# Kernel optimization log

Hardware: AMD Instinct MI355X
Metric: run time of the kernel (lower is better)

Reference implementation:

```python
import jax, jax.numpy as jnp
import numpy as np

EPS = 1e-6
NEG = -10000.0  # matches _merge_attn_masks neg_inf

def rms(x, w):
    return x * jax.lax.rsqrt(jnp.mean(x * x, axis=-1, keepdims=True) + EPS) * w

def setup_inputs() -> dict:
    key = jax.random.key(0)
    ks = jax.random.split(key, 16)
    B, Tq, Tk, D, H, G, dh, F, E = 4, 1024, 1024, 1024, 16, 4, 64, 4096, 8
    s = 1.0 / np.sqrt(D)
    sf = 1.0 / np.sqrt(F)
    return {
        "x": jax.random.normal(ks[0], (B, Tq, D), jnp.float32),
        "k_ctx": jax.random.normal(ks[1], (B, Tk, G, dh), jnp.float32),
        "v_ctx": jax.random.normal(ks[2], (B, Tk, G, dh), jnp.float32),
        "sa_norm_w": jnp.ones((D,), jnp.float32),
        "w_qkv": jax.random.normal(ks[3], (D, 3 * D), jnp.float32) * s,
        "sa_wout": jax.random.normal(ks[4], (D, D), jnp.float32) * s,
        "ca_norm_w": jnp.ones((D,), jnp.float32),
        "w_q": jax.random.normal(ks[5], (D, D), jnp.float32) * s,
        "ca_wout": jax.random.normal(ks[6], (D, D), jnp.float32) * s,
        "moe_norm_w": jnp.ones((D,), jnp.float32),
        "w_gate": jax.random.normal(ks[7], (D, E), jnp.float32) * s,
        "w1": jax.random.normal(ks[8], (E, D, F), jnp.float32) * s,
        "b1": jnp.zeros((E, F), jnp.float32),
        "w2": jax.random.normal(ks[9], (E, F, D), jnp.float32) * sf,
        "b2": jnp.zeros((E, D), jnp.float32),
    }

def _attn(q, k, v, mask=None):
    # q,k,v: [B,H,T,dh]
    dh = q.shape[-1]
    scores = jnp.einsum("bhqd,bhkd->bhqk", q, k) / jnp.sqrt(jnp.float32(dh))
    if mask is not None:
        scores = scores + mask
    p = jax.nn.softmax(scores, axis=-1)
    return jnp.einsum("bhqk,bhkd->bhqd", p, v)

def reference(x, k_ctx, v_ctx, sa_norm_w, w_qkv, sa_wout, ca_norm_w, w_q, ca_wout,
              moe_norm_w, w_gate, w1, b1, w2, b2):
    B, Tq, D = x.shape
    Tk, G, dh = k_ctx.shape[1], k_ctx.shape[2], k_ctx.shape[3]
    H = 16
    rep = H // G

    # ---- self-attention (causal, pre-norm RMS, residual) ----
    xn = rms(x, sa_norm_w)
    qkv = xn @ w_qkv  # [B,Tq,3D]
    q, k, v = jnp.split(qkv, 3, axis=-1)
    split = lambda t: t.reshape(B, Tq, H, dh).transpose(0, 2, 1, 3)
    i = jnp.arange(Tq)[:, None]
    j = jnp.arange(Tq)[None, :]
    causal = jnp.where(j <= i, 0.0, NEG).astype(jnp.float32)[None, None]
    y = _attn(split(q), split(k), split(v), causal)
    y = y.transpose(0, 2, 1, 3).reshape(B, Tq, D) @ sa_wout
    x = x + y

    # ---- cross-attention GQA ----
    qc = rms(x, ca_norm_w) @ w_q
    qc = qc.reshape(B, Tq, H, dh).transpose(0, 2, 1, 3)
    kk = jnp.repeat(k_ctx, rep, axis=2).transpose(0, 2, 1, 3)  # [B,H,Tk,dh]
    vv = jnp.repeat(v_ctx, rep, axis=2).transpose(0, 2, 1, 3)
    yc = _attn(qc, kk, vv)
    yc = yc.transpose(0, 2, 1, 3).reshape(B, Tq, D) @ ca_wout
    x = x + yc

    # ---- top-1 MoE FFN ----
    xm = rms(x, moe_norm_w)
    gate_scores = jax.nn.softmax(xm @ w_gate, axis=-1)  # [B,T,E]
    top1_idx = jnp.argmax(gate_scores, axis=-1)
    top1_score = jnp.max(gate_scores, axis=-1)
    E = w1.shape[0]
    out = jnp.zeros_like(xm)
    for e in range(E):  # small fixed expert count
        ye = jax.nn.silu(xm @ w1[e] + b1[e]) @ w2[e] + b2[e]
        out = jnp.where((top1_idx == e)[..., None], ye, out)
    out = out * top1_score[..., None]
    return x + out
```

## Files before the change

kernel.cpp:

```cpp
#include <hip/hip_runtime.h>
#include <hip/hip_bf16.h>
#include <stdint.h>

#define B_  4
#define T_  1024
#define D_  1024
#define H_  16
#define DH  64
#define F_  4096
#define E_  8
#define NT  (B_*T_)

typedef float f32x4 __attribute__((ext_vector_type(4)));
typedef short bf16x8 __attribute__((ext_vector_type(8)));
#define MFMA_BF16 __builtin_amdgcn_mfma_f32_16x16x32_bf16

union PK8 { uint32_t u[4]; bf16x8 v; };

#define GL16(gsrc, ldst)                                                      \
  __builtin_amdgcn_global_load_lds(                                           \
      (const __attribute__((address_space(1))) void*)(const void*)(gsrc),     \
      (__attribute__((address_space(3))) void*)(void*)(ldst), 16, 0, 0)

static __device__ __forceinline__ uint16_t f2bf(float f) {
  uint32_t u = __float_as_uint(f);
  u += 0x7FFFu + ((u >> 16) & 1u);
  return (uint16_t)(u >> 16);
}
static __device__ __forceinline__ void unpack8(const uint4 p0, const uint4 p1, bf16x8 &hi, bf16x8 &lo) {
  PK8 H, L;
  H.u[0] = __builtin_amdgcn_perm(p0.y, p0.x, 0x07060302u);
  L.u[0] = __builtin_amdgcn_perm(p0.y, p0.x, 0x05040100u);
  H.u[1] = __builtin_amdgcn_perm(p0.w, p0.z, 0x07060302u);
  L.u[1] = __builtin_amdgcn_perm(p0.w, p0.z, 0x05040100u);
  H.u[2] = __builtin_amdgcn_perm(p1.y, p1.x, 0x07060302u);
  L.u[2] = __builtin_amdgcn_perm(p1.y, p1.x, 0x05040100u);
  H.u[3] = __builtin_amdgcn_perm(p1.w, p1.z, 0x07060302u);
  L.u[3] = __builtin_amdgcn_perm(p1.w, p1.z, 0x05040100u);
  hi = H.v; lo = L.v;
}

__global__ __launch_bounds__(256) void k_pack_t2(const float* __restrict__ in,
                                                 uint16_t* __restrict__ outh, uint16_t* __restrict__ outl,
                                                 int K, int N) {
  __shared__ float t[32][33];
  const size_t mo = (size_t)blockIdx.z * K * N;
  in += mo; outh += mo; outl += mo;
  int n0 = blockIdx.x * 32, k0 = blockIdx.y * 32;
  int tx = threadIdx.x & 31, ty = threadIdx.x >> 5;
#pragma unroll
  for (int i = 0; i < 32; i += 8) t[ty + i][tx] = in[(size_t)(k0 + ty + i) * N + n0 + tx];
  __syncthreads();
#pragma unroll
  for (int i = 0; i < 32; i += 8) {
    float v = t[tx][ty + i];
    uint16_t h = f2bf(v);
    uint16_t l = f2bf(v - __uint_as_float((uint32_t)h << 16));
    size_t o = (size_t)(n0 + ty + i) * K + k0 + tx;
    outh[o] = h; outl[o] = l;
  }
}

__global__ __launch_bounds__(256) void k_bf_t(const float* __restrict__ in, uint16_t* __restrict__ out,
                                              int K, int N) {
  __shared__ float t[64][65];
  const size_t mo = (size_t)blockIdx.z * K * N;
  in += mo; out += mo;
  int n0 = blockIdx.x * 64, k0 = blockIdx.y * 64;
  int tr = threadIdx.x >> 4;
  int tc = (threadIdx.x & 15) * 4;
#pragma unroll
  for (int i = 0; i < 64; i += 16) {
    float4 v = *(const float4*)&in[(size_t)(k0 + tr + i) * N + n0 + tc];
    t[tr + i][tc] = v.x; t[tr + i][tc + 1] = v.y; t[tr + i][tc + 2] = v.z; t[tr + i][tc + 3] = v.w;
  }
  __syncthreads();
#pragma unroll
  for (int i = 0; i < 64; i += 16) {
    int n = tr + i;
    uint16_t b0 = f2bf(t[tc][n]), b1 = f2bf(t[tc + 1][n]);
    uint16_t b2 = f2bf(t[tc + 2][n]), b3 = f2bf(t[tc + 3][n]);
    uint2 wv;
    wv.x = ((uint32_t)b1 << 16) | b0;
    wv.y = ((uint32_t)b3 << 16) | b2;
    *(uint2*)&out[(size_t)(n0 + n) * K + k0 + tc] = wv;
  }
}

__global__ __launch_bounds__(256) void k_t16(const uint16_t* __restrict__ inh, const uint16_t* __restrict__ inl,
                                             uint16_t* __restrict__ outh, uint16_t* __restrict__ outl) {
  __shared__ uint16_t th[64][68], tl[64][68];
  int b = blockIdx.z, t0 = blockIdx.x * 64, c0 = blockIdx.y * 64;
  int tr = threadIdx.x >> 4;
  int tc = (threadIdx.x & 15) * 4;
#pragma unroll
  for (int i = 0; i < 64; i += 16) {
    size_t src = (size_t)(b * T_ + t0 + tr + i) * 3072 + 2048 + c0 + tc;
    *(uint2*)&th[tr + i][tc] = *(const uint2*)&inh[src];
    *(uint2*)&tl[tr + i][tc] = *(const uint2*)&inl[src];
  }
  __syncthreads();
#pragma unroll
  for (int i = 0; i < 64; i += 16) {
    int n = tr + i;
    size_t dst = (size_t)(b * 1024 + c0 + n) * T_ + t0 + tc;
    uint2 ph, pl;
    ph.x = ((uint32_t)th[tc + 1][n] << 16) | th[tc][n];
    ph.y = ((uint32_t)th[tc + 3][n] << 16) | th[tc + 2][n];
    pl.x = ((uint32_t)tl[tc + 1][n] << 16) | tl[tc][n];
    pl.y = ((uint32_t)tl[tc + 3][n] << 16) | tl[tc + 2][n];
    *(uint2*)&outh[dst] = ph;
    *(uint2*)&outl[dst] = pl;
  }
}

__global__ __launch_bounds__(256) void k_packf2(const float* __restrict__ in,
                                                uint16_t* __restrict__ oh, uint16_t* __restrict__ ol) {
  int i = (blockIdx.x * 256 + threadIdx.x) * 4;
  float4 v = *(const float4*)&in[i];
  uint16_t h0 = f2bf(v.x), h1 = f2bf(v.y), h2 = f2bf(v.z), h3 = f2bf(v.w);
  uint2 ph, pl;
  ph.x = ((uint32_t)h1 << 16) | h0;
  ph.y = ((uint32_t)h3 << 16) | h2;
  pl.x = ((uint32_t)f2bf(v.y - __uint_as_float((uint32_t)h1 << 16)) << 16) |
         f2bf(v.x - __uint_as_float((uint32_t)h0 << 16));
  pl.y = ((uint32_t)f2bf(v.w - __uint_as_float((uint32_t)h3 << 16)) << 16) |
         f2bf(v.z - __uint_as_float((uint32_t)h2 << 16));
  *(uint2*)&oh[i] = ph;
  *(uint2*)&ol[i] = pl;
}

__global__ __launch_bounds__(256) void k_tf32(const float* __restrict__ in,
                                              uint16_t* __restrict__ oh, uint16_t* __restrict__ ol) {
  __shared__ float t[32][33];
  int b = blockIdx.z, t0 = blockIdx.x * 32, c0 = blockIdx.y * 32;
  int tx = threadIdx.x & 31, ty = threadIdx.x >> 5;
#pragma unroll
  for (int i = 0; i < 32; i += 8)
    t[ty + i][tx] = in[(size_t)(b * T_ + t0 + ty + i) * 256 + c0 + tx];
  __syncthreads();
#pragma unroll
  for (int i = 0; i < 32; i += 8) {
    float v = t[tx][ty + i];
    uint16_t h = f2bf(v);
    size_t o = (size_t)(b * 256 + c0 + ty + i) * T_ + t0 + tx;
    oh[o] = h;
    ol[o] = f2bf(v - __uint_as_float((uint32_t)h << 16));
  }
}

__global__ __launch_bounds__(256) void k_rms(const float* __restrict__ x, const float* __restrict__ w,
                                             uint16_t* __restrict__ oh, uint16_t* __restrict__ ol,
                                             const float* __restrict__ wg, int* __restrict__ idxp,
                                             float* __restrict__ scb) {
  int row = blockIdx.x;
  const float* xr = x + (size_t)row * D_;
  int t = threadIdx.x;
  float4 xv = *(const float4*)&xr[t * 4];
  float s = xv.x * xv.x + xv.y * xv.y + xv.z * xv.z + xv.w * xv.w;
#pragma unroll
  for (int o = 32; o; o >>= 1) s += __shfl_xor(s, o, 64);
  __shared__ float ps[4];
  __shared__ float ga[4][8];
  if ((t & 63) == 0) ps[t >> 6] = s;
  __syncthreads();
  s = ps[0] + ps[1] + ps[2] + ps[3];
  float sc = 1.0f / sqrtf(s * (1.0f / (float)D_) + 1e-6f);
  float4 wv = *(const float4*)&w[t * 4];
  float o0 = xv.x * sc * wv.x, o1 = xv.y * sc * wv.y, o2 = xv.z * sc * wv.z, o3 = xv.w * sc * wv.w;
  uint16_t h0 = f2bf(o0), h1 = f2bf(o1), h2 = f2bf(o2), h3 = f2bf(o3);
  if (oh) {
    uint2 ph;
    ph.x = ((uint32_t)h1 << 16) | h0;
    ph.y = ((uint32_t)h3 << 16) | h2;
    *(uint2*)&oh[(size_t)row * D_ + t * 4] = ph;
  }
  if (ol) {
    uint16_t l0 = f2bf(o0 - __uint_as_float((uint32_t)h0 << 16));
    uint16_t l1 = f2bf(o1 - __uint_as_float((uint32_t)h1 << 16));
    uint16_t l2 = f2bf(o2 - __uint_as_float((uint32_t)h2 << 16));
    uint16_t l3 = f2bf(o3 - __uint_as_float((uint32_t)h3 << 16));
    uint2 pl;
    pl.x = ((uint32_t)l1 << 16) | l0;
    pl.y = ((uint32_t)l3 << 16) | l2;
    *(uint2*)&ol[(size_t)row * D_ + t * 4] = pl;
  }
  if (wg) {
    float a[8] = {};
    float ov[4] = {o0, o1, o2, o3};
#pragma unroll
    for (int j = 0; j < 4; j++) {
      const float* wr = &wg[(size_t)(t * 4 + j) * 8];
      float4 wa = *(const float4*)wr, wb = *(const float4*)(wr + 4);
      float v = ov[j];
      a[0] += v * wa.x; a[1] += v * wa.y; a[2] += v * wa.z; a[3] += v * wa.w;
      a[4] += v * wb.x; a[5] += v * wb.y; a[6] += v * wb.z; a[7] += v * wb.w;
    }
#pragma unroll
    for (int e = 0; e < 8; e++)
#pragma unroll
      for (int o = 32; o; o >>= 1) a[e] += __shfl_xor(a[e], o, 64);
    if ((t & 63) == 0)
#pragma unroll
      for (int e = 0; e < 8; e++) ga[t >> 6][e] = a[e];
    __syncthreads();
    if (t == 0) {
      float g[8];
#pragma unroll
      for (int e = 0; e < 8; e++) g[e] = ga[0][e] + ga[1][e] + ga[2][e] + ga[3][e];
      int bi = 0; float bv = g[0];
#pragma unroll
      for (int e = 1; e < 8; e++) if (g[e] > bv) { bv = g[e]; bi = e; }
      float se = 0.f;
#pragma unroll
      for (int e = 0; e < 8; e++) se += expf(g[e] - bv);
      idxp[row] = bi;
      scb[row] = 1.0f / se;
    }
  }
}

#define GBM 128
#define GBN 64
__global__ __launch_bounds__(256) void k_gemm_split(const uint16_t* __restrict__ Ahg, const uint16_t* __restrict__ Alg,
                                                    const uint16_t* __restrict__ Whg, const uint16_t* __restrict__ Wlg,
                                                    float* __restrict__ C, const float* __restrict__ res,
                                                    uint16_t* __restrict__ Cph, uint16_t* __restrict__ Cpl,
                                                    int scale_cols, int M, int N, int K) {
  __shared__ uint16_t Ah[2][GBM][32], Al[2][GBM][32];
  __shared__ uint16_t Wh[2][GBN][32], Wl[2][GBN][32];
  int m0 = blockIdx.y * GBM, n0 = blockIdx.x * GBN;
  int tid = threadIdx.x, wv = tid >> 6, ln = tid & 63, mi = ln & 15, b8 = ln >> 4;
  int lr = ln >> 2, lc = ln & 3;
  int cg = lc ^ (lr & 3);
  int rowA = wv * 32 + lr;
  int rowW = wv * 16 + lr;
  const uint16_t* pAh  = Ahg + (size_t)(m0 + rowA) * K + cg * 8;
  const uint16_t* pAl  = Alg + (size_t)(m0 + rowA) * K + cg * 8;
  const uint16_t* pAh2 = pAh + (size_t)16 * K;
  const uint16_t* pAl2 = pAl + (size_t)16 * K;
  const uint16_t* pWh  = Whg + (size_t)(n0 + rowW) * K + cg * 8;
  const uint16_t* pWl  = Wlg + (size_t)(n0 + rowW) * K + cg * 8;
  const int ch8 = (b8 ^ (mi & 3)) * 8;
  f32x4 acc[2][4] = {};

#define STAGE(bf) do {                                                         \
    GL16(pAh,  &Ah[bf][wv * 32][0]);                                           \
    GL16(pAh2, &Ah[bf][wv * 32 + 16][0]);                                      \
    GL16(pAl,  &Al[bf][wv * 32][0]);                                           \
    GL16(pAl2, &Al[bf][wv * 32 + 16][0]);                                      \
    GL16(pWh,  &Wh[bf][wv * 16][0]);                                           \
    GL16(pWl,  &Wl[bf][wv * 16][0]);                                           \
    pAh += 32; pAh2 += 32; pAl += 32; pAl2 += 32; pWh += 32; pWl += 32;        \
  } while (0)

  const int NK = K >> 5;
  STAGE(0);
  __syncthreads();
  int cur = 0;
  for (int t = 0; t < NK; ++t) {
    if (t + 1 < NK) STAGE(cur ^ 1);
    bf16x8 ah[2], al[2], bh[4], bl[4];
#pragma unroll
    for (int fm = 0; fm < 2; fm++) {
      ah[fm] = *(const bf16x8*)&Ah[cur][wv * 32 + fm * 16 + mi][ch8];
      al[fm] = *(const bf16x8*)&Al[cur][wv * 32 + fm * 16 + mi][ch8];
    }
#pragma unroll
    for (int fn = 0; fn < 4; fn++) {
      bh[fn] = *(const bf16x8*)&Wh[cur][fn * 16 + mi][ch8];
      bl[fn] = *(const bf16x8*)&Wl[cur][fn * 16 + mi][ch8];
    }
#pragma unroll
    for (int fm = 0; fm < 2; fm++)
#pragma unroll
      for (int fn = 0; fn < 4; fn++) {
        acc[fm][fn] = MFMA_BF16(al[fm], bh[fn], acc[fm][fn], 0, 0, 0);
        acc[fm][fn] = MFMA_BF16(ah[fm], bl[fn], acc[fm][fn], 0, 0, 0);
        acc[fm][fn] = MFMA_BF16(ah[fm], bh[fn], acc[fm][fn], 0, 0, 0);
      }
    __syncthreads();
    cur ^= 1;
  }
#undef STAGE
#pragma unroll
  for (int fm = 0; fm < 2; fm++)
#pragma unroll
    for (int fn = 0; fn < 4; fn++)
#pragma unroll
      for (int rr = 0; rr < 4; rr++) {
        int row = m0 + wv * 32 + fm * 16 + b8 * 4 + rr;
        int col = n0 + fn * 16 + mi;
        float v = acc[fm][fn][rr];
        size_t o = (size_t)row * N + col;
        if (Cph) {
          if (col < scale_cols) v *= 0.125f;
          uint16_t hv = f2bf(v);
          Cph[o] = hv;
          Cpl[o] = f2bf(v - __uint_as_float((uint32_t)hv << 16));
        } else {
          if (res) v += res[o];
          C[o] = v;
        }
      }
}

template <bool CAUSAL>
__global__ __launch_bounds__(256, 3) void k_fattn(
    const uint16_t* __restrict__ qhg, const uint16_t* __restrict__ qlg, int qs,
    const uint16_t* __restrict__ khg, const uint16_t* __restrict__ klg, int ks_, int khdiv,
    const uint16_t* __restrict__ vhg, const uint16_t* __restrict__ vlg, int nvrows,
    uint16_t* __restrict__ yhg, uint16_t* __restrict__ ylg) {
  __shared__ uint16_t Ksh[64][68], Ksl[64][68];
  __shared__ uint16_t Vsh[64][68], Vsl[64][68];
  __shared__ uint32_t Ps[4][32][36];
  const int h = blockIdx.y, b = blockIdx.z;
  const int qt = CAUSAL ? ((blockIdx.x + h + 2 * b) & 7) : blockIdx.x;
  const int tid = threadIdx.x, wv = tid >> 6, ln = tid & 63, mi = ln & 15, b8 = ln >> 4;
  const int koff = (h / khdiv) * 64;
  const uint16_t* kbh = khg + (size_t)b * T_ * ks_ + koff;
  const uint16_t* kbl = klg + (size_t)b * T_ * ks_ + koff;
  const uint16_t* vbh = vhg + ((size_t)b * nvrows + koff) * T_;
  const uint16_t* vbl = vlg + ((size_t)b * nvrows + koff) * T_;

  bf16x8 qh[2][2], ql[2][2];
#pragma unroll
  for (int u = 0; u < 2; u++)
#pragma unroll
    for (int k2 = 0; k2 < 2; k2++) {
      size_t o = (size_t)(b * T_ + qt * 128 + wv * 32 + u * 16 + mi) * qs + h * 64 + k2 * 32 + b8 * 8;
      qh[u][k2] = *(const bf16x8*)&qhg[o];
      ql[u][k2] = *(const bf16x8*)&qlg[o];
    }

  float m[2][4], l[2][4];
  f32x4 o[2][4] = {};
#pragma unroll
  for (int u = 0; u < 2; u++)
#pragma unroll
    for (int r = 0; r < 4; r++) { m[u][r] = -1e30f; l[u][r] = 0.f; }

  const int nkt = CAUSAL ? (2 * qt + 2) : (T_ / 64);
  for (int kt = 0; kt < nkt; kt++) {
    __syncthreads();
    {
      int rr = tid >> 2, cc = (tid & 3) * 16;
      size_t ko = (size_t)(kt * 64 + rr) * ks_ + cc;
      *(uint4*)&Ksh[rr][cc]     = *(const uint4*)&kbh[ko];
      *(uint4*)&Ksh[rr][cc + 8] = *(const uint4*)&kbh[ko + 8];
      *(uint4*)&Ksl[rr][cc]     = *(const uint4*)&kbl[ko];
      *(uint4*)&Ksl[rr][cc + 8] = *(const uint4*)&kbl[ko + 8];
      size_t vo = (size_t)rr * T_ + kt * 64 + cc;
      *(uint4*)&Vsh[rr][cc]     = *(const uint4*)&vbh[vo];
      *(uint4*)&Vsh[rr][cc + 8] = *(const uint4*)&vbh[vo + 8];
      *(uint4*)&Vsl[rr][cc]     = *(const uint4*)&vbl[vo];
      *(uint4*)&Vsl[rr][cc + 8] = *(const uint4*)&vbl[vo + 8];
    }
    __syncthreads();
#pragma unroll
    for (int s = 0; s < 2; s++) {
      bf16x8 kh[2][2], kl[2][2];
#pragma unroll
      for (int nf = 0; nf < 2; nf++)
#pragma unroll
        for (int k2 = 0; k2 < 2; k2++) {
          int rrow = s * 32 + nf * 16 + mi, ccol = k2 * 32 + b8 * 8;
          kh[nf][k2] = *(const bf16x8*)&Ksh[rrow][ccol];
          kl[nf][k2] = *(const bf16x8*)&Ksl[rrow][ccol];
        }
      f32x4 a[2][2] = {};
#pragma unroll
      for (int u = 0; u < 2; u++)
#pragma unroll
        for (int nf = 0; nf < 2; nf++)
#pragma unroll
          for (int k2 = 0; k2 < 2; k2++) {
            a[u][nf] = MFMA_BF16(ql[u][k2], kh[nf][k2], a[u][nf], 0, 0, 0);
            a[u][nf] = MFMA_BF16(qh[u][k2], kl[nf][k2], a[u][nf], 0, 0, 0);
            a[u][nf] = MFMA_BF16(qh[u][k2], kh[nf][k2], a[u][nf], 0, 0, 0);
          }
      if (CAUSAL && kt >= 2 * qt) {
        int kg = kt * 64 + s * 32 + mi;
#pragma unroll
        for (int u = 0; u < 2; u++) {
          int qg = qt * 128 + wv * 32 + u * 16 + b8 * 4;
#pragma unroll
          for (int r = 0; r < 4; r++) {
            if (kg > qg + r)      a[u][0][r] = -1e30f;
            if (kg + 16 > qg + r) a[u][1][r] = -1e30f;
          }
        }
      }
#pragma unroll
      for (int u = 0; u < 2; u++) {
        float pm[4];
#pragma unroll
        for (int r = 0; r < 4; r++) pm[r] = fmaxf(a[u][0][r], a[u][1][r]);
#pragma unroll
        for (int off = 1; off <= 8; off <<= 1)
#pragma unroll
          for (int r = 0; r < 4; r++) pm[r] = fmaxf(pm[r], __shfl_xor(pm[r], off, 64));
        float sc[4];
#pragma unroll
        for (int r = 0; r < 4; r++) {
          float mn = fmaxf(m[u][r], pm[r]);
          sc[r] = __expf(m[u][r] - mn);
          m[u][r] = mn;
          a[u][0][r] = __expf(a[u][0][r] - mn);
          a[u][1][r] = __expf(a[u][1][r] - mn);
        }
        float rs[4];
#pragma unroll
        for (int r = 0; r < 4; r++) rs[r] = a[u][0][r] + a[u][1][r];
#pragma unroll
        for (int off = 1; off <= 8; off <<= 1)
#pragma unroll
          for (int r = 0; r < 4; r++) rs[r] += __shfl_xor(rs[r], off, 64);
#pragma unroll
        for (int r = 0; r < 4; r++) l[u][r] = l[u][r] * sc[r] + rs[r];
#pragma unroll
        for (int f = 0; f < 4; f++)
#pragma unroll
          for (int r = 0; r < 4; r++) o[u][f][r] *= sc[r];
#pragma unroll
        for (int r = 0; r < 4; r++) {
          uint32_t Hw, Lw;
          asm("v_cvt_pk_bf16_f32 %0, %1, %2" : "=v"(Hw) : "v"(a[u][0][r]), "v"(a[u][1][r]));
          float h0 = __uint_as_float(Hw << 16);
          float h1 = __uint_as_float(Hw & 0xffff0000u);
          float r0 = a[u][0][r] - h0, r1 = a[u][1][r] - h1;
          asm("v_cvt_pk_bf16_f32 %0, %1, %2" : "=v"(Lw) : "v"(r0), "v"(r1));
          Ps[wv][u * 16 + b8 * 4 + r][mi]      = __builtin_amdgcn_perm(Hw, Lw, 0x05040100u);
          Ps[wv][u * 16 + b8 * 4 + r][16 + mi] = __builtin_amdgcn_perm(Hw, Lw, 0x07060302u);
        }
      }
      bf16x8 ph[2], pl[2];
#pragma unroll
      for (int u = 0; u < 2; u++) {
        const uint32_t* p = &Ps[wv][u * 16 + mi][b8 * 8];
        unpack8(*(const uint4*)p, *(const uint4*)(p + 4), ph[u], pl[u]);
      }
#pragma unroll
      for (int f = 0; f < 4; f++) {
        int rrow = f * 16 + mi, ccol = s * 32 + b8 * 8;
        bf16x8 vh = *(const bf16x8*)&Vsh[rrow][ccol];
        bf16x8 vl = *(const bf16x8*)&Vsl[rrow][ccol];
#pragma unroll
        for (int u = 0; u < 2; u++) {
          o[u][f] = MFMA_BF16(pl[u], vh, o[u][f], 0, 0, 0);
          o[u][f] = MFMA_BF16(ph[u], vl, o[u][f], 0, 0, 0);
          o[u][f] = MFMA_BF16(ph[u], vh, o[u][f], 0, 0, 0);
        }
      }
    }
  }
#pragma unroll
  for (int u = 0; u < 2; u++)
#pragma unroll
    for (int r = 0; r < 4; r++) {
      float inv = 1.0f / l[u][r];
      int row = qt * 128 + wv * 32 + u * 16 + b8 * 4 + r;
#pragma unroll
      for (int f = 0; f < 4; f++) {
        size_t idx = (size_t)(b * T_ + row) * D_ + h * 64 + f * 16 + mi;
        float v = o[u][f][r] * inv;
        uint16_t hv = f2bf(v);
        yhg[idx] = hv;
        ylg[idx] = f2bf(v - __uint_as_float((uint32_t)hv << 16));
      }
    }
}

__global__ __launch_bounds__(256) void k_bucket(const int* __restrict__ idx, int* __restrict__ cnt,
                                                int* __restrict__ lists) {
  int tok = blockIdx.x * 256 + threadIdx.x;
  int e = idx[tok];
  int p = atomicAdd(&cnt[e], 1);
  lists[e * NT + p] = tok;
}

__global__ __launch_bounds__(256) void k_moe1(const uint16_t* __restrict__ xmbf, const uint16_t* __restrict__ w1t,
                                              const float* __restrict__ b1, const int* __restrict__ cnt,
                                              const int* __restrict__ lists, uint16_t* __restrict__ hbf) {
  int e = blockIdx.z;
  int c = cnt[e];
  int m0 = blockIdx.y * 64;
  if (m0 >= c) return;
  int n0 = blockIdx.x * 64;
  __shared__ uint16_t As[64][72];
  __shared__ uint16_t Ws[64][72];
  __shared__ int toks[64];
  int tid = threadIdx.x, wv = tid >> 6, ln = tid & 63, mi = ln & 15, b8 = ln >> 4;
  if (tid < 64) toks[tid] = (m0 + tid < c) ? lists[e * NT + m0 + tid] : -1;
  __syncthreads();
  int r = tid >> 2, c16 = (tid & 3) * 16;
  int tk = toks[r];
  const uint16_t* asrc = (tk >= 0) ? (xmbf + (size_t)tk * D_ + c16) : nullptr;
  const uint16_t* wsrc = w1t + (size_t)e * F_ * D_ + (size_t)(n0 + r) * D_ + c16;
  f32x4 acc[4] = {};
  for (int k0 = 0; k0 < D_; k0 += 64) {
    {
      uint4 a0 = make_uint4(0, 0, 0, 0), a1 = make_uint4(0, 0, 0, 0);
      if (asrc) { a0 = *(const uint4*)(asrc + k0); a1 = *(const uint4*)(asrc + k0 + 8); }
      uint4 w0 = *(const uint4*)(wsrc + k0), w1v = *(const uint4*)(wsrc + k0 + 8);
      *(uint4*)&As[r][c16] = a0; *(uint4*)&As[r][c16 + 8] = a1;
      *(uint4*)&Ws[r][c16] = w0; *(uint4*)&Ws[r][c16 + 8] = w1v;
    }
    __syncthreads();
#pragma unroll
    for (int ks = 0; ks < 2; ks++) {
      bf16x8 a = *(const bf16x8*)&As[wv * 16 + mi][ks * 32 + b8 * 8];
#pragma unroll
      for (int fn = 0; fn < 4; fn++) {
        bf16x8 bb = *(const bf16x8*)&Ws[fn * 16 + mi][ks * 32 + b8 * 8];
        acc[fn] = MFMA_BF16(a, bb, acc[fn], 0, 0, 0);
      }
    }
    __syncthreads();
  }
#pragma unroll
  for (int fn = 0; fn < 4; fn++)
#pragma unroll
    for (int rr = 0; rr < 4; rr++) {
      int rt = wv * 16 + b8 * 4 + rr;
      if (m0 + rt < c) {
        int tok = toks[rt];
        int col = n0 + fn * 16 + mi;
        float v = acc[fn][rr] + b1[e * F_ + col];
        v = v / (1.0f + expf(-v));
        hbf[(size_t)tok * F_ + col] = f2bf(v);
      }
    }
}

__global__ __launch_bounds__(256) void k_moe2(const uint16_t* __restrict__ hbf, const uint16_t* __restrict__ w2t,
                                              const float* __restrict__ b2, const float* __restrict__ x2,
                                              const float* __restrict__ sc, const int* __restrict__ cnt,
                                              const int* __restrict__ lists, float* __restrict__ out) {
  int e = blockIdx.z;
  int c = cnt[e];
  int m0 = blockIdx.y * 64;
  if (m0 >= c) return;
  int n0 = blockIdx.x * 64;
  __shared__ uint16_t As[64][72];
  __shared__ uint16_t Ws[64][72];
  __shared__ int toks[64];
  int tid = threadIdx.x, wv = tid >> 6, ln = tid & 63, mi = ln & 15, b8 = ln >> 4;
  if (tid < 64) toks[tid] = (m0 + tid < c) ? lists[e * NT + m0 + tid] : -1;
  __syncthreads();
  int r = tid >> 2, c16 = (tid & 3) * 16;
  int tk = toks[r];
  const uint16_t* asrc = (tk >= 0) ? (hbf + (size_t)tk * F_ + c16) : nullptr;
  const uint16_t* wsrc = w2t + (size_t)e * D_ * F_ + (size_t)(n0 + r) * F_ + c16;
  f32x4 acc[4] = {};
  for (int k0 = 0; k0 < F_; k0 += 64) {
    {
      uint4 a0 = make_uint4(0, 0, 0, 0), a1 = make_uint4(0, 0, 0, 0);
      if (asrc) { a0 = *(const uint4*)(asrc + k0); a1 = *(const uint4*)(asrc + k0 + 8); }
      uint4 w0 = *(const uint4*)(wsrc + k0), w1v = *(const uint4*)(wsrc + k0 + 8);
      *(uint4*)&As[r][c16] = a0; *(uint4*)&As[r][c16 + 8] = a1;
      *(uint4*)&Ws[r][c16] = w0; *(uint4*)&Ws[r][c16 + 8] = w1v;
    }
    __syncthreads();
#pragma unroll
    for (int ks = 0; ks < 2; ks++) {
      bf16x8 a = *(const bf16x8*)&As[wv * 16 + mi][ks * 32 + b8 * 8];
#pragma unroll
      for (int fn = 0; fn < 4; fn++) {
        bf16x8 bb = *(const bf16x8*)&Ws[fn * 16 + mi][ks * 32 + b8 * 8];
        acc[fn] = MFMA_BF16(a, bb, acc[fn], 0, 0, 0);
      }
    }
    __syncthreads();
  }
#pragma unroll
  for (int fn = 0; fn < 4; fn++)
#pragma unroll
    for (int rr = 0; rr < 4; rr++) {
      int rt = wv * 16 + b8 * 4 + rr;
      if (m0 + rt < c) {
        int tok = toks[rt];
        int col = n0 + fn * 16 + mi;
        float v = acc[fn][rr] + b2[e * D_ + col];
        out[(size_t)tok * D_ + col] = x2[(size_t)tok * D_ + col] + sc[tok] * v;
      }
    }
}

extern "C" void kernel_launch(void* const* d_in, const int* in_sizes, int n_in,
                              void* d_out, int out_size, void* d_ws, size_t ws_size,
                              hipStream_t stream) {
  const float* x       = (const float*)d_in[0];
  const float* k_ctx   = (const float*)d_in[1];
  const float* v_ctx   = (const float*)d_in[2];
  const float* sa_nw   = (const float*)d_in[3];
  const float* w_qkv   = (const float*)d_in[4];
  const float* sa_wout = (const float*)d_in[5];
  const float* ca_nw   = (const float*)d_in[6];
  const float* w_q     = (const float*)d_in[7];
  const float* ca_wout = (const float*)d_in[8];
  const float* moe_nw  = (const float*)d_in[9];
  const float* w_gate  = (const float*)d_in[10];
  const float* w1      = (const float*)d_in[11];
  const float* b1      = (const float*)d_in[12];
  const float* w2      = (const float*)d_in[13];
  const float* b2      = (const float*)d_in[14];
  float* out = (float*)d_out;
  (void)in_sizes; (void)n_in; (void)out_size; (void)ws_size;

  char* ws = (char*)d_ws;
  size_t off = 0;
  auto alloc = [&](size_t bytes) { char* p = ws + off; off += (bytes + 255) & ~(size_t)255; return p; };
  uint16_t* xnh   = (uint16_t*)alloc((size_t)NT * D_ * 2);
  uint16_t* xnl   = (uint16_t*)alloc((size_t)NT * D_ * 2);
  uint16_t* yh    = (uint16_t*)alloc((size_t)NT * D_ * 2);
  uint16_t* yl    = (uint16_t*)alloc((size_t)NT * D_ * 2);
  float*    x1    = (float*)alloc((size_t)NT * D_ * 4);
  uint16_t* qkvh  = (uint16_t*)alloc((size_t)NT * 3 * D_ * 2);
  uint16_t* qkvl  = (uint16_t*)alloc((size_t)NT * 3 * D_ * 2);
  float* x2 = (float*)qkvh;
  uint16_t* qch = qkvl;
  uint16_t* qcl = qkvl + (size_t)NT * D_;
  uint16_t* wqkvTh = (uint16_t*)alloc((size_t)D_ * 3 * D_ * 2);
  uint16_t* wqkvTl = (uint16_t*)alloc((size_t)D_ * 3 * D_ * 2);
  uint16_t* sawTh  = (uint16_t*)alloc((size_t)D_ * D_ * 2);
  uint16_t* sawTl  = (uint16_t*)alloc((size_t)D_ * D_ * 2);
  uint16_t* wqTh   = (uint16_t*)alloc((size_t)D_ * D_ * 2);
  uint16_t* wqTl   = (uint16_t*)alloc((size_t)D_ * D_ * 2);
  uint16_t* cawTh  = (uint16_t*)alloc((size_t)D_ * D_ * 2);
  uint16_t* cawTl  = (uint16_t*)alloc((size_t)D_ * D_ * 2);
  uint16_t* w1t   = (uint16_t*)alloc((size_t)E_ * D_ * F_ * 2);
  uint16_t* w2t   = (uint16_t*)alloc((size_t)E_ * D_ * F_ * 2);
  uint16_t* hbf   = (uint16_t*)alloc((size_t)NT * F_ * 2);
  uint16_t* vth   = (uint16_t*)hbf;
  uint16_t* vtl   = vth + (size_t)NT * D_;
  uint16_t* kch   = (uint16_t*)((char*)hbf + (size_t)16 * 1024 * 1024);
  uint16_t* kcl   = (uint16_t*)((char*)hbf + (size_t)18 * 1024 * 1024);
  uint16_t* vcth  = (uint16_t*)((char*)hbf + (size_t)20 * 1024 * 1024);
  uint16_t* vctl  = (uint16_t*)((char*)hbf + (size_t)22 * 1024 * 1024);
  uint16_t* xmbf  = (uint16_t*)alloc((size_t)NT * D_ * 2);
  int*   idx   = (int*)alloc(NT * 4);
  float* scb   = (float*)alloc(NT * 4);
  int*   cnt   = (int*)alloc(256);
  int*   lists = (int*)alloc((size_t)E_ * NT * 4);

  k_pack_t2<<<dim3(3 * D_ / 32, D_ / 32, 1), 256, 0, stream>>>(w_qkv, wqkvTh, wqkvTl, D_, 3 * D_);
  k_pack_t2<<<dim3(D_ / 32, D_ / 32, 1), 256, 0, stream>>>(sa_wout, sawTh, sawTl, D_, D_);
  k_pack_t2<<<dim3(D_ / 32, D_ / 32, 1), 256, 0, stream>>>(w_q, wqTh, wqTl, D_, D_);
  k_pack_t2<<<dim3(D_ / 32, D_ / 32, 1), 256, 0, stream>>>(ca_wout, cawTh, cawTl, D_, D_);
  k_bf_t<<<dim3(F_ / 64, D_ / 64, E_), 256, 0, stream>>>(w1, w1t, D_, F_);
  k_bf_t<<<dim3(D_ / 64, F_ / 64, E_), 256, 0, stream>>>(w2, w2t, F_, D_);
  k_packf2<<<(B_ * T_ * 256) / 1024, 256, 0, stream>>>(k_ctx, kch, kcl);
  k_tf32<<<dim3(T_ / 32, 256 / 32, B_), 256, 0, stream>>>(v_ctx, vcth, vctl);

  k_rms<<<NT, 256, 0, stream>>>(x, sa_nw, xnh, xnl, nullptr, nullptr, nullptr);
  k_gemm_split<<<dim3(3 * D_ / GBN, NT / GBM), 256, 0, stream>>>(xnh, xnl, wqkvTh, wqkvTl, nullptr, nullptr, qkvh, qkvl, 1024, NT, 3 * D_, D_);
  k_t16<<<dim3(T_ / 64, D_ / 64, B_), 256, 0, stream>>>(qkvh, qkvl, vth, vtl);
  k_fattn<true><<<dim3(T_ / 128, H_, B_), 256, 0, stream>>>(qkvh, qkvl, 3072, qkvh + 1024, qkvl + 1024, 3072, 1, vth, vtl, 1024, yh, yl);
  k_gemm_split<<<dim3(D_ / GBN, NT / GBM), 256, 0, stream>>>(yh, yl, sawTh, sawTl, x1, x, nullptr, nullptr, 0, NT, D_, D_);

  k_rms<<<NT, 256, 0, stream>>>(x1, ca_nw, xnh, xnl, nullptr, nullptr, nullptr);
  k_gemm_split<<<dim3(D_ / GBN, NT / GBM), 256, 0, stream>>>(xnh, xnl, wqTh, wqTl, nullptr, nullptr, qch, qcl, 1024, NT, D_, D_);
  k_fattn<false><<<dim3(T_ / 128, H_, B_), 256, 0, stream>>>(qch, qcl, 1024, kch, kcl, 256, 4, vcth, vctl, 256, yh, yl);
  k_gemm_split<<<dim3(D_ / GBN, NT / GBM), 256, 0, stream>>>(yh, yl, cawTh, cawTl, x2, x1, nullptr, nullptr, 0, NT, D_, D_);

  k_rms<<<NT, 256, 0, stream>>>(x2, moe_nw, xmbf, nullptr, w_gate, idx, scb);
  hipMemsetAsync(cnt, 0, 32, stream);
  k_bucket<<<NT / 256, 256, 0, stream>>>(idx, cnt, lists);
  k_moe1<<<dim3(F_ / 64, NT / 64, E_), 256, 0, stream>>>(xmbf, w1t, b1, cnt, lists, hbf);
  k_moe2<<<dim3(D_ / 64, NT / 64, E_), 256, 0, stream>>>(hbf, w2t, b2, x2, scb, cnt, lists, out);
}
```

Before: 845.4 us.

## Merge weight-packing launches and widen MoE up-projection tile to 64x128

Four separate split-bf16 transpose launches become one kernel indexed by blockIdx.z, and the two expert-weight bf16 transposes become another, cutting launch count. The MoE first GEMM moves from a 64x64 to a 64x128 tile. Each wave now computes a 64x32 sub-tile with 4x2 MFMA accumulators and reuses A fragments across two N fragments, which lowers LDS traffic and A reloads per FLOP. The cost is more registers and LDS per block and half as many blocks, which matters when the per-expert token count is small.

```diff
diff --git a/kernel.cpp b/kernel.cpp
--- a/kernel.cpp
+++ b/kernel.cpp
@@ -40,13 +40,21 @@
   hi = H.v; lo = L.v;
 }
 
-__global__ __launch_bounds__(256) void k_pack_t2(const float* __restrict__ in,
-                                                 uint16_t* __restrict__ outh, uint16_t* __restrict__ outl,
-                                                 int K, int N) {
+__global__ __launch_bounds__(256) void k_pack_all(
+    const float* __restrict__ wqkv, const float* __restrict__ saw,
+    const float* __restrict__ wq,   const float* __restrict__ caw,
+    uint16_t* __restrict__ qkvTh, uint16_t* __restrict__ qkvTl,
+    uint16_t* __restrict__ sawTh, uint16_t* __restrict__ sawTl,
+    uint16_t* __restrict__ wqTh,  uint16_t* __restrict__ wqTl,
+    uint16_t* __restrict__ cawTh, uint16_t* __restrict__ cawTl) {
   __shared__ float t[32][33];
-  const size_t mo = (size_t)blockIdx.z * K * N;
-  in += mo; outh += mo; outl += mo;
-  int n0 = blockIdx.x * 32, k0 = blockIdx.y * 32;
+  int z = blockIdx.z;
+  const float* in; uint16_t *oh, *ol; int N, nbase;
+  if (z < 3)       { in = wqkv; oh = qkvTh; ol = qkvTl; N = 3072; nbase = z * 1024; }
+  else if (z == 3) { in = saw;  oh = sawTh; ol = sawTl; N = 1024; nbase = 0; }
+  else if (z == 4) { in = wq;   oh = wqTh;  ol = wqTl;  N = 1024; nbase = 0; }
+  else             { in = caw;  oh = cawTh; ol = cawTl; N = 1024; nbase = 0; }
+  int n0 = nbase + blockIdx.x * 32, k0 = blockIdx.y * 32;
   int tx = threadIdx.x & 31, ty = threadIdx.x >> 5;
 #pragma unroll
   for (int i = 0; i < 32; i += 8) t[ty + i][tx] = in[(size_t)(k0 + ty + i) * N + n0 + tx];
@@ -56,17 +64,25 @@
     float v = t[tx][ty + i];
     uint16_t h = f2bf(v);
     uint16_t l = f2bf(v - __uint_as_float((uint32_t)h << 16));
-    size_t o = (size_t)(n0 + ty + i) * K + k0 + tx;
-    outh[o] = h; outl[o] = l;
-  }
-}
-
-__global__ __launch_bounds__(256) void k_bf_t(const float* __restrict__ in, uint16_t* __restrict__ out,
-                                              int K, int N) {
+    size_t o = (size_t)(n0 + ty + i) * 1024 + k0 + tx;
+    oh[o] = h; ol[o] = l;
+  }
+}
+
+__global__ __launch_bounds__(256) void k_bf_t2(const float* __restrict__ w1, const float* __restrict__ w2,
+                                               uint16_t* __restrict__ w1t, uint16_t* __restrict__ w2t) {
   __shared__ float t[64][65];
-  const size_t mo = (size_t)blockIdx.z * K * N;
+  int z = blockIdx.z;
+  int which = z >> 3, e = z & 7;
+  const float* in = which ? w2 : w1;
+  uint16_t* out = which ? w2t : w1t;
+  int K = which ? F_ : D_, N = which ? D_ : F_;
+  const size_t mo = (size_t)e * (size_t)D_ * F_;
   in += mo; out += mo;
-  int n0 = blockIdx.x * 64, k0 = blockIdx.y * 64;
+  int tile = blockIdx.x;
+  int n0, k0;
+  if (which) { n0 = (tile & 15) * 64; k0 = (tile >> 4) * 64; }
+  else       { n0 = (tile & 63) * 64; k0 = (tile >> 6) * 64; }
   int tr = threadIdx.x >> 4;
   int tc = (threadIdx.x & 15) * 4;
 #pragma unroll
@@ -486,51 +502,62 @@
   int c = cnt[e];
   int m0 = blockIdx.y * 64;
   if (m0 >= c) return;
-  int n0 = blockIdx.x * 64;
+  int n0 = blockIdx.x * 128;
   __shared__ uint16_t As[64][72];
-  __shared__ uint16_t Ws[64][72];
+  __shared__ uint16_t Ws[128][72];
   __shared__ int toks[64];
   int tid = threadIdx.x, wv = tid >> 6, ln = tid & 63, mi = ln & 15, b8 = ln >> 4;
   if (tid < 64) toks[tid] = (m0 + tid < c) ? lists[e * NT + m0 + tid] : -1;
   __syncthreads();
-  int r = tid >> 2, c16 = (tid & 3) * 16;
-  int tk = toks[r];
-  const uint16_t* asrc = (tk >= 0) ? (xmbf + (size_t)tk * D_ + c16) : nullptr;
-  const uint16_t* wsrc = w1t + (size_t)e * F_ * D_ + (size_t)(n0 + r) * D_ + c16;
-  f32x4 acc[4] = {};
+  int ra = tid >> 2, ca = (tid & 3) * 16;
+  int rw = tid >> 1, cw = (tid & 1) * 32;
+  int tk = toks[ra];
+  const uint16_t* asrc = (tk >= 0) ? (xmbf + (size_t)tk * D_ + ca) : nullptr;
+  const uint16_t* wsrc = w1t + (size_t)e * F_ * D_ + (size_t)(n0 + rw) * D_ + cw;
+  f32x4 acc[4][2] = {};
   for (int k0 = 0; k0 < D_; k0 += 64) {
     {
       uint4 a0 = make_uint4(0, 0, 0, 0), a1 = make_uint4(0, 0, 0, 0);
       if (asrc) { a0 = *(const uint4*)(asrc + k0); a1 = *(const uint4*)(asrc + k0 + 8); }
-      uint4 w0 = *(const uint4*)(wsrc + k0), w1v = *(const uint4*)(wsrc + k0 + 8);
-      *(uint4*)&As[r][c16] = a0; *(uint4*)&As[r][c16 + 8] = a1;
-      *(uint4*)&Ws[r][c16] = w0; *(uint4*)&Ws[r][c16 + 8] = w1v;
+      uint4 w0 = *(const uint4*)(wsrc + k0),      w1v = *(const uint4*)(wsrc + k0 + 8);
+      uint4 w2v = *(const uint4*)(wsrc + k0 + 16), w3v = *(const uint4*)(wsrc + k0 + 24);
+      *(uint4*)&As[ra][ca] = a0;      *(uint4*)&As[ra][ca + 8] = a1;
+      *(uint4*)&Ws[rw][cw] = w0;      *(uint4*)&Ws[rw][cw + 8] = w1v;
+      *(uint4*)&Ws[rw][cw + 16] = w2v; *(uint4*)&Ws[rw][cw + 24] = w3v;
     }
     __syncthreads();
 #pragma unroll
     for (int ks = 0; ks < 2; ks++) {
-      bf16x8 a = *(const bf16x8*)&As[wv * 16 + mi][ks * 32 + b8 * 8];
-#pragma unroll
-      for (int fn = 0; fn < 4; fn++) {
-        bf16x8 bb = *(const bf16x8*)&Ws[fn * 16 + mi][ks * 32 + b8 * 8];
-        acc[fn] = MFMA_BF16(a, bb, acc[fn], 0, 0, 0);
-      }
-    }
-    __syncthreads();
-  }
-#pragma unroll
-  for (int fn = 0; fn < 4; fn++)
-#pragma unroll
-    for (int rr = 0; rr < 4; rr++) {
-      int rt = wv * 16 + b8 * 4 + rr;
-      if (m0 + rt < c) {
-        int tok = toks[rt];
-        int col = n0 + fn * 16 + mi;
-        float v = acc[fn][rr] + b1[e * F_ + col];
-        v = v / (1.0f + expf(-v));
-        hbf[(size_t)tok * F_ + col] = f2bf(v);
-      }
-    }
+      bf16x8 a[4], bb[2];
+#pragma unroll
+      for (int fm = 0; fm < 4; fm++)
+        a[fm] = *(const bf16x8*)&As[fm * 16 + mi][ks * 32 + b8 * 8];
+#pragma unroll
+      for (int nf = 0; nf < 2; nf++)
+        bb[nf] = *(const bf16x8*)&Ws[wv * 32 + nf * 16 + mi][ks * 32 + b8 * 8];
+#pragma unroll
+      for (int fm = 0; fm < 4; fm++)
+#pragma unroll
+        for (int nf = 0; nf < 2; nf++)
+          acc[fm][nf] = MFMA_BF16(a[fm], bb[nf], acc[fm][nf], 0, 0, 0);
+    }
+    __syncthreads();
+  }
+#pragma unroll
+  for (int fm = 0; fm < 4; fm++)
+#pragma unroll
+    for (int nf = 0; nf < 2; nf++)
+#pragma unroll
+      for (int rr = 0; rr < 4; rr++) {
+        int rt = fm * 16 + b8 * 4 + rr;
+        if (m0 + rt < c) {
+          int tok = toks[rt];
+          int col = n0 + wv * 32 + nf * 16 + mi;
+          float v = acc[fm][nf][rr] + b1[e * F_ + col];
+          v = v / (1.0f + expf(-v));
+          hbf[(size_t)tok * F_ + col] = f2bf(v);
+        }
+      }
 }
 
 __global__ __launch_bounds__(256) void k_moe2(const uint16_t* __restrict__ hbf, const uint16_t* __restrict__ w2t,
@@ -644,12 +671,10 @@
   int*   cnt   = (int*)alloc(256);
   int*   lists = (int*)alloc((size_t)E_ * NT * 4);
 
-  k_pack_t2<<<dim3(3 * D_ / 32, D_ / 32, 1), 256, 0, stream>>>(w_qkv, wqkvTh, wqkvTl, D_, 3 * D_);
-  k_pack_t2<<<dim3(D_ / 32, D_ / 32, 1), 256, 0, stream>>>(sa_wout, sawTh, sawTl, D_, D_);
-  k_pack_t2<<<dim3(D_ / 32, D_ / 32, 1), 256, 0, stream>>>(w_q, wqTh, wqTl, D_, D_);
-  k_pack_t2<<<dim3(D_ / 32, D_ / 32, 1), 256, 0, stream>>>(ca_wout, cawTh, cawTl, D_, D_);
-  k_bf_t<<<dim3(F_ / 64, D_ / 64, E_), 256, 0, stream>>>(w1, w1t, D_, F_);
-  k_bf_t<<<dim3(D_ / 64, F_ / 64, E_), 256, 0, stream>>>(w2, w2t, F_, D_);
+  k_pack_all<<<dim3(32, 32, 6), 256, 0, stream>>>(w_qkv, sa_wout, w_q, ca_wout,
+                                                  wqkvTh, wqkvTl, sawTh, sawTl,
+                                                  wqTh, wqTl, cawTh, cawTl);
+  k_bf_t2<<<dim3(1024, 1, 16), 256, 0, stream>>>(w1, w2, w1t, w2t);
   k_packf2<<<(B_ * T_ * 256) / 1024, 256, 0, stream>>>(k_ctx, kch, kcl);
   k_tf32<<<dim3(T_ / 32, 256 / 32, B_), 256, 0, stream>>>(v_ctx, vcth, vctl);
 
@@ -667,6 +692,6 @@
   k_rms<<<NT, 256, 0, stream>>>(x2, moe_nw, xmbf, nullptr, w_gate, idx, scb);
   hipMemsetAsync(cnt, 0, 32, stream);
   k_bucket<<<NT / 256, 256, 0, stream>>>(idx, cnt, lists);
-  k_moe1<<<dim3(F_ / 64, NT / 64, E_), 256, 0, stream>>>(xmbf, w1t, b1, cnt, lists, hbf);
+  k_moe1<<<dim3(F_ / 128, NT / 64, E_), 256, 0, stream>>>(xmbf, w1t, b1, cnt, lists, hbf);
   k_moe2<<<dim3(D_ / 64, NT / 64, E_), 256, 0, stream>>>(hbf, w2t, b2, x2, scb, cnt, lists, out);
 }
```

After: 843.2 us, median of 2. Within noise of the previous version (-0.3%).
